# Kernel optimization log

Hardware: AMD Instinct MI355X
Metric: run time of the kernel (lower is better)

The kernel has to match this reference:

```python
import jax, jax.numpy as jnp
import numpy as np
import math

D_MODEL = 1024
NUM_HEADS = 16
THETA = 10000.0


def _rope(x, theta):
    # x: [b, h, n, d_k], interleaved even/odd rotation as in the torch RoPE
    n, d_k = x.shape[-2], x.shape[-1]
    powers = jnp.arange(0, d_k, 2, dtype=jnp.float32) / d_k
    freqs = 1.0 / (theta ** powers)                       # [d_k/2]
    t = jnp.arange(n, dtype=jnp.float32)
    angles = jnp.outer(t, freqs)                          # [n, d_k/2]
    cos = jnp.cos(angles).astype(x.dtype)
    sin = jnp.sin(angles).astype(x.dtype)
    x_even = x[..., 0::2]
    x_odd = x[..., 1::2]
    rot_even = x_even * cos - x_odd * sin
    rot_odd = x_even * sin + x_odd * cos
    return jnp.stack([rot_even, rot_odd], axis=-1).reshape(x.shape)


def setup_inputs() -> dict:
    key = jax.random.key(0)
    ks = jax.random.split(key, 5)
    B, N, D = 2, 2048, D_MODEL
    std = math.sqrt(2.0 / (D + D))
    x = jax.random.normal(ks[0], (B, N, D), dtype=jnp.float32)
    wq = jax.random.normal(ks[1], (D, D), dtype=jnp.float32) * std
    wk = jax.random.normal(ks[2], (D, D), dtype=jnp.float32) * std
    wv = jax.random.normal(ks[3], (D, D), dtype=jnp.float32) * std
    wo = jax.random.normal(ks[4], (D, D), dtype=jnp.float32) * std
    return {"x": x, "wq": wq, "wk": wk, "wv": wv, "wo": wo}


def reference(x, wq, wk, wv, wo):
    B, N, D = x.shape
    H = NUM_HEADS
    d_k = D // H

    def split_heads(t):  # [b, n, d] -> [b, h, n, d_k]
        return t.reshape(B, N, H, d_k).transpose(0, 2, 1, 3)

    Q = split_heads(x @ wq.T)
    K = split_heads(x @ wk.T)
    V = split_heads(x @ wv.T)

    Q = _rope(Q, THETA)
    K = _rope(K, THETA)

    scale = 1.0 / math.sqrt(d_k)
    scores = jnp.einsum('bhqd,bhkd->bhqk', Q, K) * scale   # [b,h,n,n]
    causal_mask = jnp.triu(jnp.ones((N, N), dtype=bool), k=1)
    scores = jnp.where(causal_mask, -jnp.inf, scores)
    attn = jax.nn.softmax(scores, axis=-1)
    out = jnp.einsum('bhqk,bhkd->bhqd', attn, V)           # [b,h,n,d_k]
    out = out.transpose(0, 2, 1, 3).reshape(B, N, D)
    return out @ wo.T
```

## Files before the change

### kernel.cpp

```cpp
#include <hip/hip_runtime.h>
#include <math.h>

typedef _Float16 hv8 __attribute__((ext_vector_type(8)));
typedef _Float16 hv4 __attribute__((ext_vector_type(4)));
typedef _Float16 hv2 __attribute__((ext_vector_type(2)));
typedef float f32x4 __attribute__((ext_vector_type(4)));

#define LDS_AS(p) ((__attribute__((address_space(3))) void*)(p))
#define GLB_AS(p) ((const __attribute__((address_space(1))) void*)(p))

__device__ __forceinline__ float fexp2(float x) {
  float r;
  asm("v_exp_f32 %0, %1" : "=v"(r) : "v"(x));
  return r;
}

__global__ void prep_kernel(const float* __restrict__ x, const float* __restrict__ wq,
                            const float* __restrict__ wk, const float* __restrict__ wv,
                            const float* __restrict__ wo, _Float16* __restrict__ xb,
                            _Float16* __restrict__ wqkv, _Float16* __restrict__ wob,
                            float2* __restrict__ tab) {
  const int bid = blockIdx.x;
  if (bid < 256) {
    const int idx = bid * 256 + threadIdx.x;
    const int pos = idx >> 5, i = idx & 31;
    const float freq = exp2f((float)i * (-13.287712379549449f / 32.0f));
    float s, c;
    sincosf((float)pos * freq, &s, &c);
    tab[idx] = make_float2(c, s);
    return;
  }
  const int i = ((bid - 256) * 256 + threadIdx.x) * 4;
  const float* s;
  _Float16* d;
  int r;
  if (i < 4194304) {
    s = x; d = xb; r = i;
  } else {
    const int j = i - 4194304;
    const int seg = j >> 20;
    r = j & 1048575;
    s = (seg == 0) ? wq : (seg == 1) ? wk : (seg == 2) ? wv : wo;
    d = (seg < 3) ? (wqkv + (size_t)seg * 1048576) : wob;
  }
  const float4 v = *reinterpret_cast<const float4*>(s + r);
  hv4 o = {(_Float16)v.x, (_Float16)v.y, (_Float16)v.z, (_Float16)v.w};
  *reinterpret_cast<hv4*>(d + r) = o;
}

__global__ __launch_bounds__(256) void ropevt_kernel(_Float16* __restrict__ QKV,
                                                     const float2* __restrict__ tab,
                                                     _Float16* __restrict__ Vt) {
  __shared__ __align__(16) _Float16 Ts[64][72];
  const int bid = blockIdx.x;
  if (bid < 4096) {
    const int idx = bid * 256 + threadIdx.x;
    const int row = idx >> 8;
    const int c8 = (idx & 255) * 8;
    const int pos = row & 2047;
    const int i0 = (c8 & 63) >> 1;
    const size_t off = (size_t)row * 3072 + c8;
    hv8 v = *reinterpret_cast<const hv8*>(QKV + off);
    const float2* tp = tab + pos * 32 + i0;
    const float4 t01 = *reinterpret_cast<const float4*>(tp);
    const float4 t23 = *reinterpret_cast<const float4*>(tp + 2);
    const float c[4] = {t01.x, t01.z, t23.x, t23.z};
    const float s[4] = {t01.y, t01.w, t23.y, t23.w};
#pragma unroll
    for (int k = 0; k < 4; k++) {
      const float e = (float)v[2 * k], o = (float)v[2 * k + 1];
      v[2 * k] = (_Float16)(e * c[k] - o * s[k]);
      v[2 * k + 1] = (_Float16)(e * s[k] + o * c[k]);
    }
    *reinterpret_cast<hv8*>(QKV + off) = v;
    return;
  }
  const int t = threadIdx.x;
  const int vb = bid - 4096;
  const int n0 = (vb & 31) * 64;
  const int bh = vb >> 5;
  const int b = bh >> 4, h = bh & 15;
  const _Float16* src = QKV + (size_t)(b * 2048 + n0) * 3072 + 2048 + h * 64;
#pragma unroll
  for (int i = 0; i < 2; i++) {
    const int s = i * 256 + t, r = s >> 3, c = (s & 7) * 8;
    *reinterpret_cast<hv8*>(&Ts[r][c]) = *reinterpret_cast<const hv8*>(src + (size_t)r * 3072 + c);
  }
  __syncthreads();
  _Float16* dst = Vt + (size_t)bh * 64 * 2048 + n0;
#pragma unroll
  for (int i = 0; i < 2; i++) {
    const int s = i * 256 + t, c = s >> 3, r0 = (s & 7) * 8;
    const int base0 = (r0 & 32) + ((r0 & 8) ? 16 : 0) + ((r0 & 16) ? 4 : 0);
    hv4 o0, o1;
#pragma unroll
    for (int k = 0; k < 4; k++) { o0[k] = Ts[r0 + k][c]; o1[k] = Ts[r0 + 4 + k][c]; }
    *reinterpret_cast<hv4*>(dst + (size_t)c * 2048 + base0) = o0;
    *reinterpret_cast<hv4*>(dst + (size_t)c * 2048 + base0 + 8) = o1;
  }
}

template <int BM, typename OutT>
__global__ __launch_bounds__(256) void gemm_nt(const _Float16* __restrict__ A,
                                               const _Float16* __restrict__ B,
                                               OutT* __restrict__ C,
                                               const int M, const int N, const int K) {
  constexpr int MI = BM / 32;
  constexpr int ALOADS = BM / 32;
  __shared__ __align__(16) _Float16 As[BM * 64];
  __shared__ __align__(16) _Float16 Bs[128 * 64];
  const int t = threadIdx.x;
  const int w = t >> 6, lane = t & 63;
  const int wr = w >> 1, wc = w & 1;
  const int g = lane >> 4, lr = lane & 15;
  const int mBase = blockIdx.y * BM, nBase = blockIdx.x * 128;

  f32x4 acc[MI][4];
#pragma unroll
  for (int a = 0; a < MI; a++)
#pragma unroll
    for (int bb = 0; bb < 4; bb++) acc[a][bb] = {0.f, 0.f, 0.f, 0.f};

  for (int k0 = 0; k0 < K; k0 += 64) {
#pragma unroll
    for (int i = 0; i < ALOADS; i++) {
      const int s = i * 256 + t;
      const int r = s >> 3;
      const int cs = ((s & 7) ^ (r & 7)) * 8;
      __builtin_amdgcn_global_load_lds(GLB_AS(A + (size_t)(mBase + r) * K + k0 + cs),
                                       LDS_AS(As + s * 8), 16, 0, 0);
    }
#pragma unroll
    for (int i = 0; i < 4; i++) {
      const int s = i * 256 + t;
      const int r = s >> 3;
      const int cs = ((s & 7) ^ (r & 7)) * 8;
      __builtin_amdgcn_global_load_lds(GLB_AS(B + (size_t)(nBase + r) * K + k0 + cs),
                                       LDS_AS(Bs + s * 8), 16, 0, 0);
    }
    __syncthreads();
#pragma unroll
    for (int ks = 0; ks < 2; ks++) {
      hv8 af[MI], bfr[4];
#pragma unroll
      for (int mi = 0; mi < MI; mi++) {
        const int ra = wr * (BM / 2) + mi * 16 + lr;
        af[mi] = *reinterpret_cast<const hv8*>(As + ra * 64 + (((ks * 4 + g) ^ (ra & 7)) * 8));
      }
#pragma unroll
      for (int ni = 0; ni < 4; ni++) {
        const int rb = wc * 64 + ni * 16 + lr;
        bfr[ni] = *reinterpret_cast<const hv8*>(Bs + rb * 64 + (((ks * 4 + g) ^ (rb & 7)) * 8));
      }
#pragma unroll
      for (int mi = 0; mi < MI; mi++)
#pragma unroll
        for (int ni = 0; ni < 4; ni++)
          acc[mi][ni] = __builtin_amdgcn_mfma_f32_16x16x32_f16(af[mi], bfr[ni], acc[mi][ni], 0, 0, 0);
    }
    __syncthreads();
  }
#pragma unroll
  for (int mi = 0; mi < MI; mi++) {
#pragma unroll
    for (int j = 0; j < 4; j++) {
      const size_t row = mBase + wr * (BM / 2) + mi * 16 + g * 4 + j;
#pragma unroll
      for (int ni = 0; ni < 4; ni++) {
        const int col = nBase + wc * 64 + ni * 16 + lr;
        C[row * N + col] = (OutT)acc[mi][ni][j];
      }
    }
  }
}

__global__ __launch_bounds__(256, 4) void attn_kernel(const _Float16* __restrict__ QKV,
                                                      const _Float16* __restrict__ Vt,
                                                      _Float16* __restrict__ O) {
  __shared__ __align__(16) _Float16 Ks[2][64 * 64];
  __shared__ __align__(16) _Float16 Vs[2][64 * 64];
  const int t = threadIdx.x;
  const int w = t >> 6, lane = t & 63;
  const int g = lane >> 4, lr = lane & 15;
  const int id = blockIdx.x;
  const int j = id >> 8, r = id & 255;
  const int bh = r & 31, base = r >> 5;
  const int half = j >> 1;
  const int qt = (j & 1) ? (31 - base - 8 * half) : (base + 8 * half);
  const int m0 = qt * 64;
  const int b = bh >> 4, h = bh & 15;
  const _Float16* Qp = QKV + (size_t)b * 2048 * 3072 + h * 64;
  const _Float16* Kp = Qp + 1024;
  const _Float16* Vp = Vt + (size_t)bh * 64 * 2048;
  _Float16* Op = O + (size_t)b * 2048 * 1024 + h * 64;

  const int qg = m0 + w * 16 + lr;

  hv8 qf[2];
#pragma unroll
  for (int ks = 0; ks < 2; ks++) {
    qf[ks] = *reinterpret_cast<const hv8*>(Qp + (size_t)qg * 3072 + ks * 32 + g * 8);
    qf[ks] = qf[ks] * (_Float16)0.18033688f;
  }

  const hv8 onesf = {(_Float16)1.0f, (_Float16)1.0f, (_Float16)1.0f, (_Float16)1.0f,
                     (_Float16)1.0f, (_Float16)1.0f, (_Float16)1.0f, (_Float16)1.0f};

  auto STAGE = [&](int kv0, int bi) {
#pragma unroll
    for (int i = 0; i < 2; i++) {
      const int s = i * 256 + t;
      const int rr = s >> 3;
      const int cs = ((s & 7) ^ (rr & 7)) * 8;
      __builtin_amdgcn_global_load_lds(GLB_AS(Kp + (size_t)(kv0 + rr) * 3072 + cs),
                                       LDS_AS(&Ks[bi][s * 8]), 16, 0, 0);
      __builtin_amdgcn_global_load_lds(GLB_AS(Vp + (size_t)rr * 2048 + kv0 + cs),
                                       LDS_AS(&Vs[bi][s * 8]), 16, 0, 0);
    }
  };

  f32x4 oacc[4];
#pragma unroll
  for (int d = 0; d < 4; d++) oacc[d] = {0.f, 0.f, 0.f, 0.f};
  f32x4 lacc = {0.f, 0.f, 0.f, 0.f};
  float mst = -INFINITY;

  const int nt = qt + 1;
  STAGE(0, 0);
  int cur = 0;

  for (int tt = 0; tt < nt; tt++) {
    __syncthreads();
    if (tt + 1 < nt) STAGE((tt + 1) * 64, cur ^ 1);
    const int kv0 = tt * 64;
    const _Float16* Kb = Ks[cur];
    const _Float16* Vb = Vs[cur];

    f32x4 sf[4];
#pragma unroll
    for (int nf = 0; nf < 4; nf++) sf[nf] = {0.f, 0.f, 0.f, 0.f};
#pragma unroll
    for (int ks = 0; ks < 2; ks++)
#pragma unroll
      for (int nf = 0; nf < 4; nf++) {
        const hv8 kf = *reinterpret_cast<const hv8*>(
            Kb + (nf * 16 + lr) * 64 + (((ks * 4 + g) ^ (lr & 7)) * 8));
        sf[nf] = __builtin_amdgcn_mfma_f32_16x16x32_f16(kf, qf[ks], sf[nf], 0, 0, 0);
      }

    const bool diag = (tt == nt - 1);
    float p[4][4];
#pragma unroll
    for (int nf = 0; nf < 4; nf++)
#pragma unroll
      for (int jj = 0; jj < 4; jj++) {
        float xv = sf[nf][jj];
        if (diag && (kv0 + nf * 16 + g * 4 + jj > qg)) xv = -INFINITY;
        p[nf][jj] = xv;
      }
    float r4[4];
#pragma unroll
    for (int nf = 0; nf < 4; nf++)
      r4[nf] = fmaxf(fmaxf(p[nf][0], p[nf][1]), fmaxf(p[nf][2], p[nf][3]));
    const float rm = fmaxf(fmaxf(r4[0], r4[1]), fmaxf(r4[2], r4[3]));
    if (!__all(rm <= mst + 8.0f)) {
      float rw = fmaxf(rm, __shfl_xor(rm, 16));
      rw = fmaxf(rw, __shfl_xor(rw, 32));
      const float mn = fmaxf(mst, rw);
      const float corr = fexp2(mst - mn);
#pragma unroll
      for (int d = 0; d < 4; d++) oacc[d] *= corr;
      lacc *= corr;
      mst = mn;
    }
#pragma unroll
    for (int nf = 0; nf < 4; nf++)
#pragma unroll
      for (int jj = 0; jj < 4; jj++) p[nf][jj] = fexp2(p[nf][jj] - mst);

    hv8 pf[2];
#pragma unroll
    for (int ks = 0; ks < 2; ks++) {
      const auto c0 = __builtin_amdgcn_cvt_pkrtz(p[2 * ks][0], p[2 * ks][1]);
      const auto c1 = __builtin_amdgcn_cvt_pkrtz(p[2 * ks][2], p[2 * ks][3]);
      const auto c2 = __builtin_amdgcn_cvt_pkrtz(p[2 * ks + 1][0], p[2 * ks + 1][1]);
      const auto c3 = __builtin_amdgcn_cvt_pkrtz(p[2 * ks + 1][2], p[2 * ks + 1][3]);
      pf[ks][0] = (_Float16)c0[0]; pf[ks][1] = (_Float16)c0[1];
      pf[ks][2] = (_Float16)c1[0]; pf[ks][3] = (_Float16)c1[1];
      pf[ks][4] = (_Float16)c2[0]; pf[ks][5] = (_Float16)c2[1];
      pf[ks][6] = (_Float16)c3[0]; pf[ks][7] = (_Float16)c3[1];
    }

#pragma unroll
    for (int dblk = 0; dblk < 4; dblk++) {
      const int row = dblk * 16 + lr;
#pragma unroll
      for (int ks = 0; ks < 2; ks++) {
        const hv8 vtf = *reinterpret_cast<const hv8*>(
            Vb + row * 64 + (((ks * 4 + g) ^ (row & 7)) * 8));
        oacc[dblk] = __builtin_amdgcn_mfma_f32_16x16x32_f16(vtf, pf[ks], oacc[dblk], 0, 0, 0);
      }
    }
#pragma unroll
    for (int ks = 0; ks < 2; ks++)
      lacc = __builtin_amdgcn_mfma_f32_16x16x32_f16(onesf, pf[ks], lacc, 0, 0, 0);
    cur ^= 1;
  }

  const float inv = 1.0f / lacc[0];
#pragma unroll
  for (int dblk = 0; dblk < 4; dblk++) {
    hv4 o;
#pragma unroll
    for (int jj = 0; jj < 4; jj++) o[jj] = (_Float16)(oacc[dblk][jj] * inv);
    *reinterpret_cast<hv4*>(Op + (size_t)qg * 1024 + dblk * 16 + g * 4) = o;
  }
}

extern "C" void kernel_launch(void* const* d_in, const int* in_sizes, int n_in,
                              void* d_out, int out_size, void* d_ws, size_t ws_size,
                              hipStream_t stream) {
  const float* x = (const float*)d_in[0];
  const float* wq = (const float*)d_in[1];
  const float* wk = (const float*)d_in[2];
  const float* wv = (const float*)d_in[3];
  const float* wo = (const float*)d_in[4];
  float* out = (float*)d_out;
  char* ws = (char*)d_ws;
  const size_t MB = 1ull << 20;
  _Float16* xb   = (_Float16*)(ws + 0 * MB);
  _Float16* wqkv = (_Float16*)(ws + 8 * MB);
  _Float16* wob  = (_Float16*)(ws + 14 * MB);
  _Float16* QKV  = (_Float16*)(ws + 16 * MB);
  _Float16* Vtb  = (_Float16*)(ws + 40 * MB);
  float2*   rtab = (float2*)(ws + 48 * MB);
  _Float16* Ab   = (_Float16*)(ws + 0 * MB);

  prep_kernel<<<8448, 256, 0, stream>>>(x, wq, wk, wv, wo, xb, wqkv, wob, rtab);

  gemm_nt<128, _Float16><<<dim3(24, 32), 256, 0, stream>>>(xb, wqkv, QKV, 4096, 3072, 1024);

  ropevt_kernel<<<5120, 256, 0, stream>>>(QKV, rtab, Vtb);

  attn_kernel<<<1024, 256, 0, stream>>>(QKV, Vtb, Ab);

  gemm_nt<64, float><<<dim3(8, 64), 256, 0, stream>>>(Ab, wob, out, 4096, 1024, 1024);
}
```

Measured before the change: 113.1 us.

## Fuse RoPE and V transpose into the QKV projection GEMM epilogue

Removes the separate ropevt kernel. The QKV GEMM epilogue now applies RoPE to the Q/K columns, using a lane shuffle to fetch each pair's partner, and writes them into a compact 2048-wide QK buffer. The V columns are written directly in the transposed, permuted Vt layout. This saves a kernel launch and a full read-modify-write pass over QKV, at the cost of scattered table loads and strided stores in the GEMM epilogue.

```diff
diff --git a/kernel.cpp b/kernel.cpp
--- a/kernel.cpp
+++ b/kernel.cpp
@@ -48,55 +48,105 @@
   *reinterpret_cast<hv4*>(d + r) = o;
 }
 
-__global__ __launch_bounds__(256) void ropevt_kernel(_Float16* __restrict__ QKV,
-                                                     const float2* __restrict__ tab,
-                                                     _Float16* __restrict__ Vt) {
-  __shared__ __align__(16) _Float16 Ts[64][72];
-  const int bid = blockIdx.x;
-  if (bid < 4096) {
-    const int idx = bid * 256 + threadIdx.x;
-    const int row = idx >> 8;
-    const int c8 = (idx & 255) * 8;
-    const int pos = row & 2047;
-    const int i0 = (c8 & 63) >> 1;
-    const size_t off = (size_t)row * 3072 + c8;
-    hv8 v = *reinterpret_cast<const hv8*>(QKV + off);
-    const float2* tp = tab + pos * 32 + i0;
-    const float4 t01 = *reinterpret_cast<const float4*>(tp);
-    const float4 t23 = *reinterpret_cast<const float4*>(tp + 2);
-    const float c[4] = {t01.x, t01.z, t23.x, t23.z};
-    const float s[4] = {t01.y, t01.w, t23.y, t23.w};
-#pragma unroll
-    for (int k = 0; k < 4; k++) {
-      const float e = (float)v[2 * k], o = (float)v[2 * k + 1];
-      v[2 * k] = (_Float16)(e * c[k] - o * s[k]);
-      v[2 * k + 1] = (_Float16)(e * s[k] + o * c[k]);
-    }
-    *reinterpret_cast<hv8*>(QKV + off) = v;
-    return;
-  }
+__global__ __launch_bounds__(256) void qkv_gemm_kernel(const _Float16* __restrict__ A,
+                                                       const _Float16* __restrict__ B,
+                                                       _Float16* __restrict__ QK,
+                                                       _Float16* __restrict__ Vt,
+                                                       const float2* __restrict__ tab) {
+  constexpr int K = 1024;
+  __shared__ __align__(16) _Float16 As[128 * 64];
+  __shared__ __align__(16) _Float16 Bs[128 * 64];
   const int t = threadIdx.x;
-  const int vb = bid - 4096;
-  const int n0 = (vb & 31) * 64;
-  const int bh = vb >> 5;
-  const int b = bh >> 4, h = bh & 15;
-  const _Float16* src = QKV + (size_t)(b * 2048 + n0) * 3072 + 2048 + h * 64;
-#pragma unroll
-  for (int i = 0; i < 2; i++) {
-    const int s = i * 256 + t, r = s >> 3, c = (s & 7) * 8;
-    *reinterpret_cast<hv8*>(&Ts[r][c]) = *reinterpret_cast<const hv8*>(src + (size_t)r * 3072 + c);
-  }
-  __syncthreads();
-  _Float16* dst = Vt + (size_t)bh * 64 * 2048 + n0;
-#pragma unroll
-  for (int i = 0; i < 2; i++) {
-    const int s = i * 256 + t, c = s >> 3, r0 = (s & 7) * 8;
-    const int base0 = (r0 & 32) + ((r0 & 8) ? 16 : 0) + ((r0 & 16) ? 4 : 0);
-    hv4 o0, o1;
-#pragma unroll
-    for (int k = 0; k < 4; k++) { o0[k] = Ts[r0 + k][c]; o1[k] = Ts[r0 + 4 + k][c]; }
-    *reinterpret_cast<hv4*>(dst + (size_t)c * 2048 + base0) = o0;
-    *reinterpret_cast<hv4*>(dst + (size_t)c * 2048 + base0 + 8) = o1;
+  const int w = t >> 6, lane = t & 63;
+  const int wr = w >> 1, wc = w & 1;
+  const int g = lane >> 4, lr = lane & 15;
+  const int mBase = blockIdx.y * 128, nBase = blockIdx.x * 128;
+
+  f32x4 acc[4][4];
+#pragma unroll
+  for (int a = 0; a < 4; a++)
+#pragma unroll
+    for (int bb = 0; bb < 4; bb++) acc[a][bb] = {0.f, 0.f, 0.f, 0.f};
+
+  for (int k0 = 0; k0 < K; k0 += 64) {
+#pragma unroll
+    for (int i = 0; i < 4; i++) {
+      const int s = i * 256 + t;
+      const int r = s >> 3;
+      const int cs = ((s & 7) ^ (r & 7)) * 8;
+      __builtin_amdgcn_global_load_lds(GLB_AS(A + (size_t)(mBase + r) * K + k0 + cs),
+                                       LDS_AS(As + s * 8), 16, 0, 0);
+    }
+#pragma unroll
+    for (int i = 0; i < 4; i++) {
+      const int s = i * 256 + t;
+      const int r = s >> 3;
+      const int cs = ((s & 7) ^ (r & 7)) * 8;
+      __builtin_amdgcn_global_load_lds(GLB_AS(B + (size_t)(nBase + r) * K + k0 + cs),
+                                       LDS_AS(Bs + s * 8), 16, 0, 0);
+    }
+    __syncthreads();
+#pragma unroll
+    for (int ks = 0; ks < 2; ks++) {
+      hv8 af[4], bfr[4];
+#pragma unroll
+      for (int mi = 0; mi < 4; mi++) {
+        const int ra = wr * 64 + mi * 16 + lr;
+        af[mi] = *reinterpret_cast<const hv8*>(As + ra * 64 + (((ks * 4 + g) ^ (ra & 7)) * 8));
+      }
+#pragma unroll
+      for (int ni = 0; ni < 4; ni++) {
+        const int rb = wc * 64 + ni * 16 + lr;
+        bfr[ni] = *reinterpret_cast<const hv8*>(Bs + rb * 64 + (((ks * 4 + g) ^ (rb & 7)) * 8));
+      }
+#pragma unroll
+      for (int mi = 0; mi < 4; mi++)
+#pragma unroll
+        for (int ni = 0; ni < 4; ni++)
+          acc[mi][ni] = __builtin_amdgcn_mfma_f32_16x16x32_f16(af[mi], bfr[ni], acc[mi][ni], 0, 0, 0);
+    }
+    __syncthreads();
+  }
+
+  const int rowBase = mBase + wr * 64;
+  const int colBase = nBase + wc * 64;
+  if (nBase < 2048) {
+    const float sgn = (lr & 1) ? 1.0f : -1.0f;
+#pragma unroll
+    for (int mi = 0; mi < 4; mi++) {
+#pragma unroll
+      for (int j = 0; j < 4; j++) {
+        const int row = rowBase + mi * 16 + g * 4 + j;
+        const int pos = row & 2047;
+#pragma unroll
+        for (int ni = 0; ni < 4; ni++) {
+          const int col = colBase + ni * 16 + lr;
+          const float2 cs2 = tab[pos * 32 + ((col & 63) >> 1)];
+          const float v = acc[mi][ni][j];
+          const float pv = __shfl_xor(v, 1);
+          QK[(size_t)row * 2048 + col] = (_Float16)(v * cs2.x + pv * (sgn * cs2.y));
+        }
+      }
+    }
+  } else {
+    const int b = rowBase >> 11;
+    const int tok0 = rowBase & 2047;
+#pragma unroll
+    for (int ni = 0; ni < 4; ni++) {
+      const int cc = colBase - 2048 + ni * 16 + lr;
+      const int h = cc >> 6, d = cc & 63;
+      _Float16* vp = Vt + ((size_t)(b * 16 + h) * 64 + d) * 2048 + tok0 + g * 8;
+      hv8 o1, o2;
+#pragma unroll
+      for (int j = 0; j < 4; j++) {
+        o1[j] = (_Float16)acc[0][ni][j];
+        o1[4 + j] = (_Float16)acc[1][ni][j];
+        o2[j] = (_Float16)acc[2][ni][j];
+        o2[4 + j] = (_Float16)acc[3][ni][j];
+      }
+      *reinterpret_cast<hv8*>(vp) = o1;
+      *reinterpret_cast<hv8*>(vp + 32) = o2;
+    }
   }
 }
 
@@ -174,7 +224,7 @@
   }
 }
 
-__global__ __launch_bounds__(256, 4) void attn_kernel(const _Float16* __restrict__ QKV,
+__global__ __launch_bounds__(256, 4) void attn_kernel(const _Float16* __restrict__ QK,
                                                       const _Float16* __restrict__ Vt,
                                                       _Float16* __restrict__ O) {
   __shared__ __align__(16) _Float16 Ks[2][64 * 64];
@@ -189,7 +239,7 @@
   const int qt = (j & 1) ? (31 - base - 8 * half) : (base + 8 * half);
   const int m0 = qt * 64;
   const int b = bh >> 4, h = bh & 15;
-  const _Float16* Qp = QKV + (size_t)b * 2048 * 3072 + h * 64;
+  const _Float16* Qp = QK + (size_t)b * 2048 * 2048 + h * 64;
   const _Float16* Kp = Qp + 1024;
   const _Float16* Vp = Vt + (size_t)bh * 64 * 2048;
   _Float16* Op = O + (size_t)b * 2048 * 1024 + h * 64;
@@ -199,7 +249,7 @@
   hv8 qf[2];
 #pragma unroll
   for (int ks = 0; ks < 2; ks++) {
-    qf[ks] = *reinterpret_cast<const hv8*>(Qp + (size_t)qg * 3072 + ks * 32 + g * 8);
+    qf[ks] = *reinterpret_cast<const hv8*>(Qp + (size_t)qg * 2048 + ks * 32 + g * 8);
     qf[ks] = qf[ks] * (_Float16)0.18033688f;
   }
 
@@ -212,7 +262,7 @@
       const int s = i * 256 + t;
       const int rr = s >> 3;
       const int cs = ((s & 7) ^ (rr & 7)) * 8;
-      __builtin_amdgcn_global_load_lds(GLB_AS(Kp + (size_t)(kv0 + rr) * 3072 + cs),
+      __builtin_amdgcn_global_load_lds(GLB_AS(Kp + (size_t)(kv0 + rr) * 2048 + cs),
                                        LDS_AS(&Ks[bi][s * 8]), 16, 0, 0);
       __builtin_amdgcn_global_load_lds(GLB_AS(Vp + (size_t)rr * 2048 + kv0 + cs),
                                        LDS_AS(&Vs[bi][s * 8]), 16, 0, 0);
@@ -331,18 +381,16 @@
   _Float16* xb   = (_Float16*)(ws + 0 * MB);
   _Float16* wqkv = (_Float16*)(ws + 8 * MB);
   _Float16* wob  = (_Float16*)(ws + 14 * MB);
-  _Float16* QKV  = (_Float16*)(ws + 16 * MB);
-  _Float16* Vtb  = (_Float16*)(ws + 40 * MB);
-  float2*   rtab = (float2*)(ws + 48 * MB);
+  _Float16* QKb  = (_Float16*)(ws + 16 * MB);
+  _Float16* Vtb  = (_Float16*)(ws + 32 * MB);
+  float2*   rtab = (float2*)(ws + 40 * MB);
   _Float16* Ab   = (_Float16*)(ws + 0 * MB);
 
   prep_kernel<<<8448, 256, 0, stream>>>(x, wq, wk, wv, wo, xb, wqkv, wob, rtab);
 
-  gemm_nt<128, _Float16><<<dim3(24, 32), 256, 0, stream>>>(xb, wqkv, QKV, 4096, 3072, 1024);
-
-  ropevt_kernel<<<5120, 256, 0, stream>>>(QKV, rtab, Vtb);
-
-  attn_kernel<<<1024, 256, 0, stream>>>(QKV, Vtb, Ab);
+  qkv_gemm_kernel<<<dim3(24, 32), 256, 0, stream>>>(xb, wqkv, QKb, Vtb, rtab);
+
+  attn_kernel<<<1024, 256, 0, stream>>>(QKb, Vtb, Ab);
 
   gemm_nt<64, float><<<dim3(8, 64), 256, 0, stream>>>(Ab, wob, out, 4096, 1024, 1024);
 }
```

Result: no change. 113.6 us (+0.5%).
